# Kernel optimization log

Hardware: AMD Instinct MI355X
Metric: run time of the kernel (lower is better)

Reference implementation:

```python
import jax, jax.numpy as jnp
import numpy as np
import math

B, T, O, D, H, L, FF = 2, 1024, 512, 1024, 16, 4, 4096
MAX_SEQ = 1024


def _ln(x, g, b, eps=1e-5):
    m = jnp.mean(x, -1, keepdims=True)
    v = jnp.mean((x - m) ** 2, -1, keepdims=True)
    return (x - m) * jax.lax.rsqrt(v + eps) * g + b


def _gelu(x):
    return jax.nn.gelu(x, approximate=False)  # torch nn.GELU default = exact erf


def setup_inputs() -> dict:
    key = jax.random.key(0)
    ks = iter(jax.random.split(key, 64))
    std = 0.02
    def w(shape):
        return (jax.random.normal(next(ks), shape, jnp.float32) * std)
    d = {
        'obs': jax.random.normal(next(ks), (B, T, O), jnp.float32),
        # encoder MLP: Linear(O,D), LN, GELU, Linear(D,D), GELU, Linear(D,D), LN
        'enc_w1': w((O, D)), 'enc_b1': jnp.zeros((D,)),
        'enc_g1': jnp.ones((D,)), 'enc_be1': jnp.zeros((D,)),
        'enc_w2': w((D, D)), 'enc_b2': jnp.zeros((D,)),
        'enc_w3': w((D, D)), 'enc_b3': jnp.zeros((D,)),
        'enc_g2': jnp.ones((D,)), 'enc_be2': jnp.zeros((D,)),
        'pos_emb': w((MAX_SEQ, D)),
        # stacked per-layer transformer params [L, ...]
        'ln1_g': jnp.ones((L, D)), 'ln1_b': jnp.zeros((L, D)),
        'wq': w((L, D, D)), 'bq': jnp.zeros((L, D)),
        'wk': w((L, D, D)), 'bk': jnp.zeros((L, D)),
        'wv': w((L, D, D)), 'bv': jnp.zeros((L, D)),
        'wo': w((L, D, D)), 'bo': jnp.zeros((L, D)),
        'ln2_g': jnp.ones((L, D)), 'ln2_b': jnp.zeros((L, D)),
        'mlp_w1': w((L, D, FF)), 'mlp_b1': jnp.zeros((L, FF)),
        'mlp_w2': w((L, FF, D)), 'mlp_b2': jnp.zeros((L, D)),
        'lnf_g': jnp.ones((D,)), 'lnf_b': jnp.zeros((D,)),
        'dec_w': w((D, O)), 'dec_b': jnp.zeros((O,)),
    }
    return d


def reference(obs, enc_w1, enc_b1, enc_g1, enc_be1, enc_w2, enc_b2, enc_w3, enc_b3,
              enc_g2, enc_be2, pos_emb, ln1_g, ln1_b, wq, bq, wk, bk, wv, bv, wo, bo,
              ln2_g, ln2_b, mlp_w1, mlp_b1, mlp_w2, mlp_b2, lnf_g, lnf_b, dec_w, dec_b):
    b, t, _ = obs.shape
    dh = D // H
    scale = 1.0 / math.sqrt(dh)
    # embedder MLP
    h = _gelu(_ln(obs @ enc_w1 + enc_b1, enc_g1, enc_be1))
    h = _gelu(h @ enc_w2 + enc_b2)
    h = _ln(h @ enc_w3 + enc_b3, enc_g2, enc_be2)
    x = h + pos_emb[:t]
    # causal mask [t, t]
    mask = jnp.tril(jnp.ones((t, t), bool))

    def block(x, p):
        g1, b1, Wq, Bq, Wk, Bk, Wv, Bv, Wo, Bo, g2, b2, W1, B1, W2, B2 = p
        hn = _ln(x, g1, b1)
        q = (hn @ Wq + Bq).reshape(b, t, H, dh).transpose(0, 2, 1, 3)
        k = (hn @ Wk + Bk).reshape(b, t, H, dh).transpose(0, 2, 1, 3)
        v = (hn @ Wv + Bv).reshape(b, t, H, dh).transpose(0, 2, 1, 3)
        att = jnp.einsum('bhtd,bhsd->bhts', q, k) * scale
        att = jnp.where(mask, att, -jnp.inf)
        att = jax.nn.softmax(att, axis=-1)
        y = jnp.einsum('bhts,bhsd->bhtd', att, v)
        y = y.transpose(0, 2, 1, 3).reshape(b, t, D)
        x = x + y @ Wo + Bo
        hm = _ln(x, g2, b2)
        x = x + _gelu(hm @ W1 + B1) @ W2 + B2
        return x, None

    stacked = (ln1_g, ln1_b, wq, bq, wk, bk, wv, bv, wo, bo,
               ln2_g, ln2_b, mlp_w1, mlp_b1, mlp_w2, mlp_b2)
    x, _ = jax.lax.scan(block, x, stacked)
    x = _ln(x, lnf_g, lnf_b)
    out_obs = x @ dec_w + dec_b
    return x, out_obs
```

## Files before the change

### kernel.cpp

```cpp
#include <hip/hip_runtime.h>
#include <utility>

typedef unsigned short u16;
typedef __bf16  bf16x8 __attribute__((ext_vector_type(8)));
typedef float   f32x4  __attribute__((ext_vector_type(4)));
typedef unsigned short u16x4 __attribute__((ext_vector_type(4)));

constexpr int Bc = 2, Tc = 1024, Oc = 512, Dc = 1024, Hc = 16, Lc = 4, FFc = 4096;
constexpr int Mc = Bc * Tc;
constexpr int Sq = 3 * Dc;

__device__ __forceinline__ u16 f2b(float f) {
    unsigned u = __float_as_uint(f);
    u = (u + 0x7fffu + ((u >> 16) & 1u)) >> 16;
    return (u16)u;
}
__device__ __forceinline__ float gelu_f(float x) {
    return 0.5f * x * (1.0f + erff(x * 0.7071067811865476f));
}

typedef const __attribute__((address_space(1))) void* gas_p;
typedef __attribute__((address_space(3))) void* las_p;
__device__ __forceinline__ void gload16(const void* g, void* l) {
    __builtin_amdgcn_global_load_lds((gas_p)g, (las_p)l, 16, 0, 0);
}

__global__ __launch_bounds__(256) void wtrans(const float* __restrict__ in,
                                              u16* __restrict__ out, int R, int C,
                                              long inBatch, long outBatch) {
    __shared__ float t[32][33];
    const float* inp = in + (size_t)blockIdx.z * inBatch;
    u16* outp = out + (size_t)blockIdx.z * outBatch;
    const int tx = threadIdx.x & 31, ty = threadIdx.x >> 5;
    const int br = blockIdx.y * 32, bc = blockIdx.x * 32;
#pragma unroll
    for (int i = 0; i < 32; i += 8)
        t[ty + i][tx] = inp[(size_t)(br + ty + i) * C + bc + tx];
    __syncthreads();
#pragma unroll
    for (int i = 0; i < 32; i += 8)
        outp[(size_t)(bc + ty + i) * R + br + tx] = f2b(t[tx][ty + i]);
}

__global__ __launch_bounds__(256) void btrans(const u16* __restrict__ in,
                                              u16* __restrict__ out, int inStride) {
    __shared__ u16 t[32][33];
    const u16* inp = in + (size_t)blockIdx.z * Tc * inStride;
    u16* outp = out + (size_t)blockIdx.z * Dc * Tc;
    const int tx = threadIdx.x & 31, ty = threadIdx.x >> 5;
    const int br = blockIdx.y * 32, bc = blockIdx.x * 32;
#pragma unroll
    for (int i = 0; i < 32; i += 8)
        t[ty + i][tx] = inp[(size_t)(br + ty + i) * inStride + bc + tx];
    __syncthreads();
#pragma unroll
    for (int i = 0; i < 32; i += 8)
        outp[(size_t)(bc + ty + i) * Tc + br + tx] = t[tx][ty + i];
}

__global__ __launch_bounds__(256) void cvt_bf(const float* __restrict__ in,
                                              u16* __restrict__ out, int n) {
    int i = blockIdx.x * 256 + threadIdx.x;
    if (i * 4 >= n) return;
    float4 v = ((const float4*)in)[i];
    u16x4 r;
    r[0] = f2b(v.x); r[1] = f2b(v.y); r[2] = f2b(v.z); r[3] = f2b(v.w);
    ((u16x4*)out)[i] = r;
}

__global__ __launch_bounds__(256) void pack_qkv_bias(const float* __restrict__ bq,
    const float* __restrict__ bk, const float* __restrict__ bv, float* __restrict__ out) {
    int i = blockIdx.x * 256 + threadIdx.x;
    int l = i / Sq, j = i % Sq;
    float v = (j < Dc) ? bq[l * Dc + j] : (j < 2 * Dc ? bk[l * Dc + j - Dc] : bv[l * Dc + j - 2 * Dc]);
    out[i] = v;
}

__global__ __launch_bounds__(256) void red2(const float* __restrict__ p,
    const float* __restrict__ bias, const float* __restrict__ resid,
    float* __restrict__ outf, int MN) {
    const int i = blockIdx.x * 256 + threadIdx.x;
    const f32x4 a = ((const f32x4*)p)[i];
    const f32x4 b = ((const f32x4*)(p + MN))[i];
    const int col4 = i & (Dc / 4 - 1);
    const f32x4 bb = ((const f32x4*)bias)[col4];
    const f32x4 r  = ((const f32x4*)resid)[i];
    f32x4 o;
#pragma unroll
    for (int j = 0; j < 4; ++j) o[j] = a[j] + b[j] + bb[j] + r[j];
    ((f32x4*)outf)[i] = o;
}

__global__ __launch_bounds__(256) void ln_kernel(
    const float* __restrict__ in, const float* __restrict__ gam,
    const float* __restrict__ bet, const float* __restrict__ pos,
    float* __restrict__ outf, u16* __restrict__ outb, int do_gelu) {
    const int row = blockIdx.x, tid = threadIdx.x;
    const float4 v = ((const float4*)(in + (size_t)row * Dc))[tid];
    float s  = v.x + v.y + v.z + v.w;
    float ss = v.x * v.x + v.y * v.y + v.z * v.z + v.w * v.w;
#pragma unroll
    for (int m = 1; m < 64; m <<= 1) {
        s  += __shfl_xor(s,  m, 64);
        ss += __shfl_xor(ss, m, 64);
    }
    __shared__ float red[8];
    const int w = tid >> 6;
    if ((tid & 63) == 0) { red[w] = s; red[4 + w] = ss; }
    __syncthreads();
    s  = red[0] + red[1] + red[2] + red[3];
    ss = red[4] + red[5] + red[6] + red[7];
    const float mean = s * (1.0f / Dc);
    const float rstd = rsqrtf(ss * (1.0f / Dc) - mean * mean + 1e-5f);
    const float4 gv = ((const float4*)gam)[tid];
    const float4 bv = ((const float4*)bet)[tid];
    float y0 = (v.x - mean) * rstd * gv.x + bv.x;
    float y1 = (v.y - mean) * rstd * gv.y + bv.y;
    float y2 = (v.z - mean) * rstd * gv.z + bv.z;
    float y3 = (v.w - mean) * rstd * gv.w + bv.w;
    if (do_gelu) { y0 = gelu_f(y0); y1 = gelu_f(y1); y2 = gelu_f(y2); y3 = gelu_f(y3); }
    if (pos) {
        const float4 pv = ((const float4*)(pos + (size_t)(row & (Tc - 1)) * Dc))[tid];
        y0 += pv.x; y1 += pv.y; y2 += pv.z; y3 += pv.w;
    }
    if (outf) {
        float4 o; o.x = y0; o.y = y1; o.z = y2; o.w = y3;
        ((float4*)(outf + (size_t)row * Dc))[tid] = o;
    }
    if (outb) {
        u16x4 r; r[0] = f2b(y0); r[1] = f2b(y1); r[2] = f2b(y2); r[3] = f2b(y3);
        ((u16x4*)(outb + (size_t)row * Dc))[tid] = r;
    }
}

template<int BM, int BN, int FM, int FN, int WM, int WN, int OCC>
__global__ __launch_bounds__(256, OCC) void gemm_k(
    const u16* __restrict__ A, const u16* __restrict__ Bt,
    const float* __restrict__ bias, const float* resid,
    float* Cf, u16* Cb, int M, int N, int Kst, int Kl, int do_gelu) {
    __shared__ u16 sA[2][BM][64];
    __shared__ u16 sB[2][BN][64];
    constexpr int NA = BM / 32;
    constexpr int NB = BN / 32;
    const int tid = threadIdx.x;
    const int lane = tid & 63, w = tid >> 6;
    const int lr = lane & 15, g = lane >> 4;
    const int wm = w / WN, wn = w % WN;

    A  += (size_t)blockIdx.z * Kl;
    Bt += (size_t)blockIdx.z * Kl;
    Cf += (size_t)blockIdx.z * M * N;

    const int gx = gridDim.x;
    const int nwg = gx * gridDim.y;
    const int orig = blockIdx.y * gx + blockIdx.x;
    const int wgid = (orig & 7) * (nwg >> 3) + (orig >> 3);
    const int s = wgid >> 6, q = wgid & 63;
    const int nsx = gx >> 3;
    const int sy = s / nsx, sx = s - sy * nsx;
    const int by = sy * 8 + (q >> 3), bx = sx * 8 + (q & 7);
    const long m0 = (long)by * BM, n0 = (long)bx * BN;

    const f32x4 fzero = {0.f, 0.f, 0.f, 0.f};
    f32x4 acc[FM][FN];
#pragma unroll
    for (int i = 0; i < FM; ++i)
#pragma unroll
        for (int j = 0; j < FN; ++j) acc[i][j] = fzero;

    const int nt = Kl / 64;
    const int srow = lane >> 3, scc = lane & 7;
    const u16* pa[NA];
    const u16* pb[NB];
#pragma unroll
    for (int r = 0; r < NA; ++r)
        pa[r] = A + (size_t)(m0 + r * 32 + w * 8 + srow) * Kst + ((scc ^ srow) * 8);
#pragma unroll
    for (int r = 0; r < NB; ++r)
        pb[r] = Bt + (size_t)(n0 + r * 32 + w * 8 + srow) * Kst + ((scc ^ srow) * 8);

    auto stage = [&](auto curc, int t) {
        constexpr int cu = decltype(curc)::value;
        if (t < nt) {
#pragma unroll
            for (int r = 0; r < NA; ++r) { gload16(pa[r], &sA[cu][r * 32 + w * 8][0]); pa[r] += 64; }
#pragma unroll
            for (int r = 0; r < NB; ++r) { gload16(pb[r], &sB[cu][r * 32 + w * 8][0]); pb[r] += 64; }
        }
    };
    auto compute = [&](auto curc) {
        constexpr int cu = decltype(curc)::value;
#pragma unroll
        for (int ks = 0; ks < 2; ++ks) {
            bf16x8 fa[FM], fb[FN];
#pragma unroll
            for (int mi = 0; mi < FM; ++mi) {
                int row = wm * (16 * FM) + mi * 16 + lr;
                fa[mi] = *(const bf16x8*)&sA[cu][row][((ks * 4 + g) ^ (row & 7)) * 8];
            }
#pragma unroll
            for (int ni = 0; ni < FN; ++ni) {
                int row = wn * (16 * FN) + ni * 16 + lr;
                fb[ni] = *(const bf16x8*)&sB[cu][row][((ks * 4 + g) ^ (row & 7)) * 8];
            }
#pragma unroll
            for (int mi = 0; mi < FM; ++mi)
#pragma unroll
                for (int ni = 0; ni < FN; ++ni)
                    acc[mi][ni] = __builtin_amdgcn_mfma_f32_16x16x32_bf16(
                        fa[mi], fb[ni], acc[mi][ni], 0, 0, 0);
        }
    };
    auto drain_barrier = [&]() {
        asm volatile("s_waitcnt vmcnt(0)" ::: "memory");
        __builtin_amdgcn_sched_barrier(0);
        __syncthreads();
    };

    std::integral_constant<int, 0> c0;
    std::integral_constant<int, 1> c1;
    stage(c0, 0);
    drain_barrier();
    for (int t = 0; t < nt; t += 2) {
        stage(c1, t + 1);
        compute(c0);
        drain_barrier();
        stage(c0, t + 2);
        compute(c1);
        drain_barrier();
    }
#pragma unroll
    for (int mi = 0; mi < FM; ++mi) {
#pragma unroll
        for (int ni = 0; ni < FN; ++ni) {
            const long nc = n0 + wn * (16 * FN) + ni * 16 + lr;
            const float bvv = bias ? bias[nc] : 0.0f;
#pragma unroll
            for (int j = 0; j < 4; ++j) {
                const long mr = m0 + wm * (16 * FM) + mi * 16 + g * 4 + j;
                float v = acc[mi][ni][j] + bvv;
                if (resid) v += resid[(size_t)mr * N + nc];
                if (do_gelu) v = gelu_f(v);
                if (Cf) Cf[(size_t)mr * N + nc] = v;
                if (Cb) Cb[(size_t)mr * N + nc] = f2b(v);
            }
        }
    }
}

__global__ __launch_bounds__(256, 2) void attn_kernel(
    const u16* __restrict__ qkv, const u16* __restrict__ Vt, u16* __restrict__ Yg) {
    __shared__ u16 sK[64][64];
    __shared__ u16 sV[64][64];
    __shared__ u16 sP[4][16][64];
    const int tid = threadIdx.x, w = tid >> 6, lane = tid & 63;
    const int lr = lane & 15, g = lane >> 4;
    const int hw = blockIdx.x;
    const int xcd = hw & 7, slot = hw >> 3;
    const int bh = xcd + 8 * (slot >> 4);
    const int qc = slot & 15;
    const int h = bh & 15, b = bh >> 4;
    const int tq0 = qc * 64 + w * 16;
    const u16* Qp = qkv + (size_t)b * Tc * Sq + h * 64;
    const u16* Kp = qkv + (size_t)b * Tc * Sq + Dc + h * 64;
    const u16* Vp = Vt + ((size_t)b * Dc + h * 64) * Tc;

    bf16x8 qf[2];
#pragma unroll
    for (int ks = 0; ks < 2; ++ks)
        qf[ks] = *(const bf16x8*)(Qp + (size_t)(tq0 + lr) * Sq + ks * 32 + g * 8);

    const f32x4 fzero = {0.f, 0.f, 0.f, 0.f};
    f32x4 o[4];
    float mst[4], lst[4];
#pragma unroll
    for (int j = 0; j < 4; ++j) { mst[j] = -1e30f; lst[j] = 0.f; }
#pragma unroll
    for (int ni = 0; ni < 4; ++ni) o[ni] = fzero;

    for (int jk = 0; jk <= qc; ++jk) {
#pragma unroll
        for (int i = 0; i < 2; ++i) {
            int c = tid + 256 * i;
            int row = c >> 3, cc = c & 7;
            *(bf16x8*)&sK[row][(cc ^ (row & 7)) * 8] =
                *(const bf16x8*)(Kp + (size_t)(jk * 64 + row) * Sq + cc * 8);
            *(bf16x8*)&sV[row][(cc ^ (row & 7)) * 8] =
                *(const bf16x8*)(Vp + (size_t)row * Tc + jk * 64 + cc * 8);
        }
        __syncthreads();
        f32x4 s[4];
#pragma unroll
        for (int ni = 0; ni < 4; ++ni) {
            const int row = ni * 16 + lr;
            bf16x8 kf0 = *(const bf16x8*)&sK[row][((0 + g) ^ (lr & 7)) * 8];
            bf16x8 kf1 = *(const bf16x8*)&sK[row][((4 + g) ^ (lr & 7)) * 8];
            s[ni] = __builtin_amdgcn_mfma_f32_16x16x32_bf16(qf[0], kf0, fzero, 0, 0, 0);
            s[ni] = __builtin_amdgcn_mfma_f32_16x16x32_bf16(qf[1], kf1, s[ni], 0, 0, 0);
        }
#pragma unroll
        for (int ni = 0; ni < 4; ++ni)
#pragma unroll
            for (int j = 0; j < 4; ++j) {
                float v = s[ni][j] * 0.125f;
                int tk = jk * 64 + ni * 16 + lr;
                int tq = tq0 + g * 4 + j;
                if (tk > tq) v = -1e30f;
                s[ni][j] = v;
            }
        float fs[4];
#pragma unroll
        for (int j = 0; j < 4; ++j) {
            float pm = fmaxf(fmaxf(s[0][j], s[1][j]), fmaxf(s[2][j], s[3][j]));
            pm = fmaxf(pm, __shfl_xor(pm, 1, 16));
            pm = fmaxf(pm, __shfl_xor(pm, 2, 16));
            pm = fmaxf(pm, __shfl_xor(pm, 4, 16));
            pm = fmaxf(pm, __shfl_xor(pm, 8, 16));
            const float m2 = fmaxf(mst[j], pm);
            fs[j] = __expf(mst[j] - m2);
#pragma unroll
            for (int ni = 0; ni < 4; ++ni)
                s[ni][j] = __expf(s[ni][j] - m2);
            float rsum = s[0][j] + s[1][j] + s[2][j] + s[3][j];
            rsum += __shfl_xor(rsum, 1, 16);
            rsum += __shfl_xor(rsum, 2, 16);
            rsum += __shfl_xor(rsum, 4, 16);
            rsum += __shfl_xor(rsum, 8, 16);
            lst[j] = lst[j] * fs[j] + rsum;
            mst[j] = m2;
        }
#pragma unroll
        for (int ni = 0; ni < 4; ++ni)
#pragma unroll
            for (int j = 0; j < 4; ++j) o[ni][j] *= fs[j];
#pragma unroll
        for (int ni = 0; ni < 4; ++ni)
#pragma unroll
            for (int j = 0; j < 4; ++j) {
                int row = g * 4 + j;
                int col = ni * 16 + lr;
                sP[w][row][(((col >> 3) ^ (row & 7)) << 3) | (col & 7)] = f2b(s[ni][j]);
            }
#pragma unroll
        for (int ks = 0; ks < 2; ++ks) {
            bf16x8 pf = *(const bf16x8*)&sP[w][lr][((ks * 4 + g) ^ (lr & 7)) * 8];
#pragma unroll
            for (int ni = 0; ni < 4; ++ni) {
                const int row = ni * 16 + lr;
                bf16x8 vf = *(const bf16x8*)&sV[row][((ks * 4 + g) ^ (lr & 7)) * 8];
                o[ni] = __builtin_amdgcn_mfma_f32_16x16x32_bf16(pf, vf, o[ni], 0, 0, 0);
            }
        }
        __syncthreads();
    }
#pragma unroll
    for (int ni = 0; ni < 4; ++ni)
#pragma unroll
        for (int j = 0; j < 4; ++j) {
            int tq = tq0 + g * 4 + j;
            int col = h * 64 + ni * 16 + lr;
            Yg[(size_t)(b * Tc + tq) * Dc + col] = f2b(o[ni][j] / lst[j]);
        }
}

extern "C" void kernel_launch(void* const* d_in, const int* in_sizes, int n_in,
                              void* d_out, int out_size, void* d_ws, size_t ws_size,
                              hipStream_t stream) {
    const float* obs    = (const float*)d_in[0];
    const float* enc_w1 = (const float*)d_in[1];
    const float* enc_b1 = (const float*)d_in[2];
    const float* enc_g1 = (const float*)d_in[3];
    const float* enc_be1= (const float*)d_in[4];
    const float* enc_w2 = (const float*)d_in[5];
    const float* enc_b2 = (const float*)d_in[6];
    const float* enc_w3 = (const float*)d_in[7];
    const float* enc_b3 = (const float*)d_in[8];
    const float* enc_g2 = (const float*)d_in[9];
    const float* enc_be2= (const float*)d_in[10];
    const float* pos_emb= (const float*)d_in[11];
    const float* ln1_g  = (const float*)d_in[12];
    const float* ln1_b  = (const float*)d_in[13];
    const float* wq     = (const float*)d_in[14];
    const float* bq     = (const float*)d_in[15];
    const float* wk     = (const float*)d_in[16];
    const float* bk     = (const float*)d_in[17];
    const float* wv     = (const float*)d_in[18];
    const float* bv     = (const float*)d_in[19];
    const float* wo     = (const float*)d_in[20];
    const float* bo     = (const float*)d_in[21];
    const float* ln2_g  = (const float*)d_in[22];
    const float* ln2_b  = (const float*)d_in[23];
    const float* mlp_w1 = (const float*)d_in[24];
    const float* mlp_b1 = (const float*)d_in[25];
    const float* mlp_w2 = (const float*)d_in[26];
    const float* mlp_b2 = (const float*)d_in[27];
    const float* lnf_g  = (const float*)d_in[28];
    const float* lnf_b  = (const float*)d_in[29];
    const float* dec_w  = (const float*)d_in[30];
    const float* dec_b  = (const float*)d_in[31];

    float* out_x = (float*)d_out;
    float* out_o = out_x + (size_t)Mc * Dc;

    char* base = (char*)d_ws;
    size_t off = 0;
    auto ab = [&](size_t e) -> u16* {
        u16* r = (u16*)(base + off); off += (e * 2 + 255) & ~(size_t)255; return r; };
    auto af = [&](size_t e) -> float* {
        float* r = (float*)(base + off); off += (e * 4 + 255) & ~(size_t)255; return r; };

    u16* wt_e1   = ab((size_t)Dc * Oc);
    u16* wt_e2   = ab((size_t)Dc * Dc);
    u16* wt_e3   = ab((size_t)Dc * Dc);
    u16* wtqkv   = ab((size_t)Lc * 3 * Dc * Dc);
    u16* wto     = ab((size_t)Lc * Dc * Dc);
    u16* wtm1    = ab((size_t)Lc * Dc * FFc);
    u16* wtm2    = ab((size_t)Lc * FFc * Dc);
    u16* wt_d    = ab((size_t)Oc * Dc);
    float* qkvb  = af((size_t)Lc * Sq);

    u16*   obs_bf = ab((size_t)Mc * Oc);
    float* tmpf   = af((size_t)Mc * Dc);
    float* xf     = af((size_t)Mc * Dc);
    float* x2f    = af((size_t)Mc * Dc);
    u16*   hn_bf  = ab((size_t)Mc * Dc);
    u16*   qkv    = ab((size_t)Mc * Sq);
    u16*   vT     = ab((size_t)Mc * Dc);
    u16*   y_bf   = ab((size_t)Mc * Dc);
    u16*   ff_bf  = ab((size_t)Mc * FFc);
    float* pk     = af((size_t)2 * Mc * Dc);

    wtrans<<<dim3(Dc / 32, Oc / 32, 1), 256, 0, stream>>>(enc_w1, wt_e1, Oc, Dc, 0, 0);
    wtrans<<<dim3(Dc / 32, Dc / 32, 1), 256, 0, stream>>>(enc_w2, wt_e2, Dc, Dc, 0, 0);
    wtrans<<<dim3(Dc / 32, Dc / 32, 1), 256, 0, stream>>>(enc_w3, wt_e3, Dc, Dc, 0, 0);
    wtrans<<<dim3(Dc / 32, Dc / 32, Lc), 256, 0, stream>>>(wq, wtqkv,            Dc, Dc, (long)Dc * Dc, (long)3 * Dc * Dc);
    wtrans<<<dim3(Dc / 32, Dc / 32, Lc), 256, 0, stream>>>(wk, wtqkv + Dc * Dc,  Dc, Dc, (long)Dc * Dc, (long)3 * Dc * Dc);
    wtrans<<<dim3(Dc / 32, Dc / 32, Lc), 256, 0, stream>>>(wv, wtqkv + 2 * Dc * Dc, Dc, Dc, (long)Dc * Dc, (long)3 * Dc * Dc);
    wtrans<<<dim3(Dc / 32, Dc / 32, Lc), 256, 0, stream>>>(wo, wto, Dc, Dc, (long)Dc * Dc, (long)Dc * Dc);
    wtrans<<<dim3(FFc / 32, Dc / 32, Lc), 256, 0, stream>>>(mlp_w1, wtm1, Dc, FFc, (long)Dc * FFc, (long)Dc * FFc);
    wtrans<<<dim3(Dc / 32, FFc / 32, Lc), 256, 0, stream>>>(mlp_w2, wtm2, FFc, Dc, (long)Dc * FFc, (long)Dc * FFc);
    wtrans<<<dim3(Oc / 32, Dc / 32, 1), 256, 0, stream>>>(dec_w, wt_d, Dc, Oc, 0, 0);
    pack_qkv_bias<<<dim3(Lc * Sq / 256), 256, 0, stream>>>(bq, bk, bv, qkvb);
    cvt_bf<<<dim3((Mc * Oc / 4 + 255) / 256), 256, 0, stream>>>(obs, obs_bf, Mc * Oc);

    auto g128 = [&](const u16* A, const u16* Bt, const float* bias, const float* resid,
                    float* Cf, u16* Cb, int M, int N, int K, int gel) {
        gemm_k<128, 128, 4, 4, 2, 2, 2><<<dim3(N / 128, M / 128), 256, 0, stream>>>(
            A, Bt, bias, resid, Cf, Cb, M, N, K, K, gel);
    };
    auto g64 = [&](const u16* A, const u16* Bt, const float* bias, const float* resid,
                   float* Cf, u16* Cb, int M, int N, int K, int gel) {
        gemm_k<64, 64, 2, 2, 2, 2, 4><<<dim3(N / 64, M / 64), 256, 0, stream>>>(
            A, Bt, bias, resid, Cf, Cb, M, N, K, K, gel);
    };
    auto lnk = [&](const float* in, const float* gg, const float* bb, const float* pos,
                   float* outf, u16* outb, int gel) {
        ln_kernel<<<dim3(Mc), 256, 0, stream>>>(in, gg, bb, pos, outf, outb, gel);
    };

    g64(obs_bf, wt_e1, enc_b1, nullptr, tmpf, nullptr, Mc, Dc, Oc, 0);
    lnk(tmpf, enc_g1, enc_be1, nullptr, nullptr, hn_bf, 1);
    g64(hn_bf, wt_e2, enc_b2, nullptr, nullptr, y_bf, Mc, Dc, Dc, 1);
    g64(y_bf, wt_e3, enc_b3, nullptr, tmpf, nullptr, Mc, Dc, Dc, 0);
    lnk(tmpf, enc_g2, enc_be2, pos_emb, xf, nullptr, 0);

    for (int l = 0; l < Lc; ++l) {
        lnk(xf, ln1_g + (size_t)l * Dc, ln1_b + (size_t)l * Dc, nullptr, nullptr, hn_bf, 0);
        g128(hn_bf, wtqkv + (size_t)l * 3 * Dc * Dc, qkvb + (size_t)l * Sq, nullptr,
             nullptr, qkv, Mc, Sq, Dc, 0);
        btrans<<<dim3(Dc / 32, Tc / 32, Bc), 256, 0, stream>>>(qkv + 2 * Dc, vT, Sq);
        attn_kernel<<<dim3(Bc * Hc * (Tc / 64)), 256, 0, stream>>>(qkv, vT, y_bf);
        g64(y_bf, wto + (size_t)l * Dc * Dc, bo + (size_t)l * Dc, xf, x2f, nullptr, Mc, Dc, Dc, 0);
        lnk(x2f, ln2_g + (size_t)l * Dc, ln2_b + (size_t)l * Dc, nullptr, nullptr, hn_bf, 0);
        g128(hn_bf, wtm1 + (size_t)l * Dc * FFc, mlp_b1 + (size_t)l * FFc, nullptr,
             nullptr, ff_bf, Mc, FFc, Dc, 1);
        gemm_k<64, 64, 2, 2, 2, 2, 4><<<dim3(Dc / 64, Mc / 64, 2), 256, 0, stream>>>(
            ff_bf, wtm2 + (size_t)l * FFc * Dc, nullptr, nullptr, pk, nullptr,
            Mc, Dc, FFc, FFc / 2, 0);
        red2<<<dim3(Mc * Dc / 4 / 256), 256, 0, stream>>>(
            pk, mlp_b2 + (size_t)l * Dc, x2f, xf, Mc * Dc);
    }

    lnk(xf, lnf_g, lnf_b, nullptr, out_x, hn_bf, 0);
    g64(hn_bf, wt_d, dec_b, nullptr, out_o, nullptr, Mc, Oc, Dc, 0);
}
```

Before: 781.5 us.

## Fuse V transpose into QKV GEMM, residual-reduce with LN, double-buffer attention KV

The QKV GEMM epilogue now writes the V columns straight into the transposed vT layout, which removes the separate btrans kernel. The split-K reduce for the MLP output is fused with the next layer's LN1, or with the final LN, in a new red2_ln kernel, saving one launch and one pass over the activation per layer. The attention kernel now double-buffers K/V tiles in shared memory, prefetching the next tile into registers while the current one is computed. It also reverses the query-chunk order so the longest causal blocks launch first. The V epilogue stores are scattered with stride Tc, which may coalesce poorly.

```diff
diff --git a/kernel.cpp b/kernel.cpp
--- a/kernel.cpp
+++ b/kernel.cpp
@@ -42,22 +42,6 @@
         outp[(size_t)(bc + ty + i) * R + br + tx] = f2b(t[tx][ty + i]);
 }
 
-__global__ __launch_bounds__(256) void btrans(const u16* __restrict__ in,
-                                              u16* __restrict__ out, int inStride) {
-    __shared__ u16 t[32][33];
-    const u16* inp = in + (size_t)blockIdx.z * Tc * inStride;
-    u16* outp = out + (size_t)blockIdx.z * Dc * Tc;
-    const int tx = threadIdx.x & 31, ty = threadIdx.x >> 5;
-    const int br = blockIdx.y * 32, bc = blockIdx.x * 32;
-#pragma unroll
-    for (int i = 0; i < 32; i += 8)
-        t[ty + i][tx] = inp[(size_t)(br + ty + i) * inStride + bc + tx];
-    __syncthreads();
-#pragma unroll
-    for (int i = 0; i < 32; i += 8)
-        outp[(size_t)(bc + ty + i) * Tc + br + tx] = t[tx][ty + i];
-}
-
 __global__ __launch_bounds__(256) void cvt_bf(const float* __restrict__ in,
                                               u16* __restrict__ out, int n) {
     int i = blockIdx.x * 256 + threadIdx.x;
@@ -74,21 +58,6 @@
     int l = i / Sq, j = i % Sq;
     float v = (j < Dc) ? bq[l * Dc + j] : (j < 2 * Dc ? bk[l * Dc + j - Dc] : bv[l * Dc + j - 2 * Dc]);
     out[i] = v;
-}
-
-__global__ __launch_bounds__(256) void red2(const float* __restrict__ p,
-    const float* __restrict__ bias, const float* __restrict__ resid,
-    float* __restrict__ outf, int MN) {
-    const int i = blockIdx.x * 256 + threadIdx.x;
-    const f32x4 a = ((const f32x4*)p)[i];
-    const f32x4 b = ((const f32x4*)(p + MN))[i];
-    const int col4 = i & (Dc / 4 - 1);
-    const f32x4 bb = ((const f32x4*)bias)[col4];
-    const f32x4 r  = ((const f32x4*)resid)[i];
-    f32x4 o;
-#pragma unroll
-    for (int j = 0; j < 4; ++j) o[j] = a[j] + b[j] + bb[j] + r[j];
-    ((f32x4*)outf)[i] = o;
 }
 
 __global__ __launch_bounds__(256) void ln_kernel(
@@ -133,11 +102,53 @@
     }
 }
 
+__global__ __launch_bounds__(256) void red2_ln(
+    const float* __restrict__ p, const float* __restrict__ bias,
+    const float* __restrict__ resid, float* __restrict__ xfout,
+    const float* __restrict__ gam, const float* __restrict__ bet,
+    float* __restrict__ lnoutf, u16* __restrict__ lnoutb) {
+    const int row = blockIdx.x, tid = threadIdx.x;
+    const f32x4 a  = ((const f32x4*)(p + (size_t)row * Dc))[tid];
+    const f32x4 b  = ((const f32x4*)(p + (size_t)Mc * Dc + (size_t)row * Dc))[tid];
+    const f32x4 bb = ((const f32x4*)bias)[tid];
+    const f32x4 r  = ((const f32x4*)(resid + (size_t)row * Dc))[tid];
+    f32x4 v;
+#pragma unroll
+    for (int j = 0; j < 4; ++j) v[j] = a[j] + b[j] + bb[j] + r[j];
+    ((f32x4*)(xfout + (size_t)row * Dc))[tid] = v;
+    float s  = v[0] + v[1] + v[2] + v[3];
+    float ss = v[0]*v[0] + v[1]*v[1] + v[2]*v[2] + v[3]*v[3];
+#pragma unroll
+    for (int m = 1; m < 64; m <<= 1) {
+        s  += __shfl_xor(s,  m, 64);
+        ss += __shfl_xor(ss, m, 64);
+    }
+    __shared__ float red[8];
+    const int w = tid >> 6;
+    if ((tid & 63) == 0) { red[w] = s; red[4 + w] = ss; }
+    __syncthreads();
+    s  = red[0] + red[1] + red[2] + red[3];
+    ss = red[4] + red[5] + red[6] + red[7];
+    const float mean = s * (1.0f / Dc);
+    const float rstd = rsqrtf(ss * (1.0f / Dc) - mean * mean + 1e-5f);
+    const f32x4 gv = ((const f32x4*)gam)[tid];
+    const f32x4 bv = ((const f32x4*)bet)[tid];
+    f32x4 y;
+#pragma unroll
+    for (int j = 0; j < 4; ++j) y[j] = (v[j] - mean) * rstd * gv[j] + bv[j];
+    if (lnoutf) ((f32x4*)(lnoutf + (size_t)row * Dc))[tid] = y;
+    u16x4 o;
+#pragma unroll
+    for (int j = 0; j < 4; ++j) o[j] = f2b(y[j]);
+    ((u16x4*)(lnoutb + (size_t)row * Dc))[tid] = o;
+}
+
 template<int BM, int BN, int FM, int FN, int WM, int WN, int OCC>
 __global__ __launch_bounds__(256, OCC) void gemm_k(
     const u16* __restrict__ A, const u16* __restrict__ Bt,
     const float* __restrict__ bias, const float* resid,
-    float* Cf, u16* Cb, int M, int N, int Kst, int Kl, int do_gelu) {
+    float* Cf, u16* Cb, u16* vTout, int vcol0,
+    int M, int N, int Kst, int Kl, int do_gelu) {
     __shared__ u16 sA[2][BM][64];
     __shared__ u16 sB[2][BN][64];
     constexpr int NA = BM / 32;
@@ -241,8 +252,13 @@
                 float v = acc[mi][ni][j] + bvv;
                 if (resid) v += resid[(size_t)mr * N + nc];
                 if (do_gelu) v = gelu_f(v);
-                if (Cf) Cf[(size_t)mr * N + nc] = v;
-                if (Cb) Cb[(size_t)mr * N + nc] = f2b(v);
+                if (vTout && nc >= vcol0) {
+                    const long d = nc - vcol0, t = mr & (Tc - 1), bb = mr >> 10;
+                    vTout[((size_t)bb * Dc + d) * Tc + t] = f2b(v);
+                } else {
+                    if (Cf) Cf[(size_t)mr * N + nc] = v;
+                    if (Cb) Cb[(size_t)mr * N + nc] = f2b(v);
+                }
             }
         }
     }
@@ -250,15 +266,15 @@
 
 __global__ __launch_bounds__(256, 2) void attn_kernel(
     const u16* __restrict__ qkv, const u16* __restrict__ Vt, u16* __restrict__ Yg) {
-    __shared__ u16 sK[64][64];
-    __shared__ u16 sV[64][64];
+    __shared__ u16 sK[2][64][64];
+    __shared__ u16 sV[2][64][64];
     __shared__ u16 sP[4][16][64];
     const int tid = threadIdx.x, w = tid >> 6, lane = tid & 63;
     const int lr = lane & 15, g = lane >> 4;
     const int hw = blockIdx.x;
     const int xcd = hw & 7, slot = hw >> 3;
     const int bh = xcd + 8 * (slot >> 4);
-    const int qc = slot & 15;
+    const int qc = 15 - (slot & 15);
     const int h = bh & 15, b = bh >> 4;
     const int tq0 = qc * 64 + w * 16;
     const u16* Qp = qkv + (size_t)b * Tc * Sq + h * 64;
@@ -278,23 +294,35 @@
 #pragma unroll
     for (int ni = 0; ni < 4; ++ni) o[ni] = fzero;
 
+    const int c0 = tid, c1 = tid + 256;
+    const int row0 = c0 >> 3, cc0 = c0 & 7;
+    const int row1 = c1 >> 3, cc1 = c1 & 7;
+    bf16x8 kr[2], vr[2];
+    auto kvload = [&](int jk) {
+        kr[0] = *(const bf16x8*)(Kp + (size_t)(jk * 64 + row0) * Sq + cc0 * 8);
+        kr[1] = *(const bf16x8*)(Kp + (size_t)(jk * 64 + row1) * Sq + cc1 * 8);
+        vr[0] = *(const bf16x8*)(Vp + (size_t)row0 * Tc + jk * 64 + cc0 * 8);
+        vr[1] = *(const bf16x8*)(Vp + (size_t)row1 * Tc + jk * 64 + cc1 * 8);
+    };
+    auto kvwrite = [&](int buf) {
+        *(bf16x8*)&sK[buf][row0][(cc0 ^ (row0 & 7)) * 8] = kr[0];
+        *(bf16x8*)&sK[buf][row1][(cc1 ^ (row1 & 7)) * 8] = kr[1];
+        *(bf16x8*)&sV[buf][row0][(cc0 ^ (row0 & 7)) * 8] = vr[0];
+        *(bf16x8*)&sV[buf][row1][(cc1 ^ (row1 & 7)) * 8] = vr[1];
+    };
+
+    kvload(0);
+    kvwrite(0);
+    __syncthreads();
     for (int jk = 0; jk <= qc; ++jk) {
-#pragma unroll
-        for (int i = 0; i < 2; ++i) {
-            int c = tid + 256 * i;
-            int row = c >> 3, cc = c & 7;
-            *(bf16x8*)&sK[row][(cc ^ (row & 7)) * 8] =
-                *(const bf16x8*)(Kp + (size_t)(jk * 64 + row) * Sq + cc * 8);
-            *(bf16x8*)&sV[row][(cc ^ (row & 7)) * 8] =
-                *(const bf16x8*)(Vp + (size_t)row * Tc + jk * 64 + cc * 8);
-        }
-        __syncthreads();
+        const int cur = jk & 1;
+        if (jk < qc) kvload(jk + 1);
         f32x4 s[4];
 #pragma unroll
         for (int ni = 0; ni < 4; ++ni) {
             const int row = ni * 16 + lr;
-            bf16x8 kf0 = *(const bf16x8*)&sK[row][((0 + g) ^ (lr & 7)) * 8];
-            bf16x8 kf1 = *(const bf16x8*)&sK[row][((4 + g) ^ (lr & 7)) * 8];
+            bf16x8 kf0 = *(const bf16x8*)&sK[cur][row][((0 + g) ^ (lr & 7)) * 8];
+            bf16x8 kf1 = *(const bf16x8*)&sK[cur][row][((4 + g) ^ (lr & 7)) * 8];
             s[ni] = __builtin_amdgcn_mfma_f32_16x16x32_bf16(qf[0], kf0, fzero, 0, 0, 0);
             s[ni] = __builtin_amdgcn_mfma_f32_16x16x32_bf16(qf[1], kf1, s[ni], 0, 0, 0);
         }
@@ -347,10 +375,11 @@
 #pragma unroll
             for (int ni = 0; ni < 4; ++ni) {
                 const int row = ni * 16 + lr;
-                bf16x8 vf = *(const bf16x8*)&sV[row][((ks * 4 + g) ^ (lr & 7)) * 8];
+                bf16x8 vf = *(const bf16x8*)&sV[cur][row][((ks * 4 + g) ^ (lr & 7)) * 8];
                 o[ni] = __builtin_amdgcn_mfma_f32_16x16x32_bf16(pf, vf, o[ni], 0, 0, 0);
             }
         }
+        if (jk < qc) kvwrite(cur ^ 1);
         __syncthreads();
     }
 #pragma unroll
@@ -444,14 +473,15 @@
     cvt_bf<<<dim3((Mc * Oc / 4 + 255) / 256), 256, 0, stream>>>(obs, obs_bf, Mc * Oc);
 
     auto g128 = [&](const u16* A, const u16* Bt, const float* bias, const float* resid,
-                    float* Cf, u16* Cb, int M, int N, int K, int gel) {
+                    float* Cf, u16* Cb, u16* vTout, int vcol0,
+                    int M, int N, int K, int gel) {
         gemm_k<128, 128, 4, 4, 2, 2, 2><<<dim3(N / 128, M / 128), 256, 0, stream>>>(
-            A, Bt, bias, resid, Cf, Cb, M, N, K, K, gel);
+            A, Bt, bias, resid, Cf, Cb, vTout, vcol0, M, N, K, K, gel);
     };
     auto g64 = [&](const u16* A, const u16* Bt, const float* bias, const float* resid,
                    float* Cf, u16* Cb, int M, int N, int K, int gel) {
         gemm_k<64, 64, 2, 2, 2, 2, 4><<<dim3(N / 64, M / 64), 256, 0, stream>>>(
-            A, Bt, bias, resid, Cf, Cb, M, N, K, K, gel);
+            A, Bt, bias, resid, Cf, Cb, nullptr, 0, M, N, K, K, gel);
     };
     auto lnk = [&](const float* in, const float* gg, const float* bb, const float* pos,
                    float* outf, u16* outb, int gel) {
@@ -464,23 +494,30 @@
     g64(y_bf, wt_e3, enc_b3, nullptr, tmpf, nullptr, Mc, Dc, Dc, 0);
     lnk(tmpf, enc_g2, enc_be2, pos_emb, xf, nullptr, 0);
 
+    lnk(xf, ln1_g, ln1_b, nullptr, nullptr, hn_bf, 0);
+
     for (int l = 0; l < Lc; ++l) {
-        lnk(xf, ln1_g + (size_t)l * Dc, ln1_b + (size_t)l * Dc, nullptr, nullptr, hn_bf, 0);
         g128(hn_bf, wtqkv + (size_t)l * 3 * Dc * Dc, qkvb + (size_t)l * Sq, nullptr,
-             nullptr, qkv, Mc, Sq, Dc, 0);
-        btrans<<<dim3(Dc / 32, Tc / 32, Bc), 256, 0, stream>>>(qkv + 2 * Dc, vT, Sq);
+             nullptr, qkv, vT, 2 * Dc, Mc, Sq, Dc, 0);
         attn_kernel<<<dim3(Bc * Hc * (Tc / 64)), 256, 0, stream>>>(qkv, vT, y_bf);
         g64(y_bf, wto + (size_t)l * Dc * Dc, bo + (size_t)l * Dc, xf, x2f, nullptr, Mc, Dc, Dc, 0);
         lnk(x2f, ln2_g + (size_t)l * Dc, ln2_b + (size_t)l * Dc, nullptr, nullptr, hn_bf, 0);
         g128(hn_bf, wtm1 + (size_t)l * Dc * FFc, mlp_b1 + (size_t)l * FFc, nullptr,
-             nullptr, ff_bf, Mc, FFc, Dc, 1);
+             nullptr, ff_bf, nullptr, 0, Mc, FFc, Dc, 1);
         gemm_k<64, 64, 2, 2, 2, 2, 4><<<dim3(Dc / 64, Mc / 64, 2), 256, 0, stream>>>(
             ff_bf, wtm2 + (size_t)l * FFc * Dc, nullptr, nullptr, pk, nullptr,
-            Mc, Dc, FFc, FFc / 2, 0);
-        red2<<<dim3(Mc * Dc / 4 / 256), 256, 0, stream>>>(
-            pk, mlp_b2 + (size_t)l * Dc, x2f, xf, Mc * Dc);
-    }
-
-    lnk(xf, lnf_g, lnf_b, nullptr, out_x, hn_bf, 0);
+            nullptr, 0, Mc, Dc, FFc, FFc / 2, 0);
+        if (l < Lc - 1) {
+            red2_ln<<<dim3(Mc), 256, 0, stream>>>(
+                pk, mlp_b2 + (size_t)l * Dc, x2f, xf,
+                ln1_g + (size_t)(l + 1) * Dc, ln1_b + (size_t)(l + 1) * Dc,
+                nullptr, hn_bf);
+        } else {
+            red2_ln<<<dim3(Mc), 256, 0, stream>>>(
+                pk, mlp_b2 + (size_t)l * Dc, x2f, xf,
+                lnf_g, lnf_b, out_x, hn_bf);
+        }
+    }
+
     g64(hn_bf, wt_d, dec_b, nullptr, out_o, nullptr, Mc, Oc, Dc, 0);
 }
```

Result: slower. 802.5 us (+2.7%).
